# Optimization experiments

Measured on AMD Instinct MI355X. Metric: run time of the kernel, lower is better.

## Reference

```python
import jax, jax.numpy as jnp
import numpy as np

TOKENS, D_IN, D_OUT = 16384, 2048, 2048


def setup_inputs() -> dict:
    key = jax.random.key(0)
    k1, k2, k3 = jax.random.split(key, 3)
    x = jax.random.normal(k1, (TOKENS, D_IN), dtype=jnp.float32)
    # int8 quantized weight, stored transposed as [in_features, out_features]
    weight = jax.random.randint(k2, (D_IN, D_OUT), -128, 128).astype(jnp.int8)
    # per-output-channel dequant scale, shape [1, out_features]
    scale = (jax.random.uniform(k3, (1, D_OUT), dtype=jnp.float32) * 0.01 + 1e-4)
    return {"x": x, "scale": scale, "weight": weight}


def reference(x, scale, weight):
    # x: [N, in], weight: int8 [in, out] (pre-transposed), scale: [1, out]
    tokens = x.shape[:-1]
    xf = x.reshape(-1, x.shape[-1])
    # cast int8 weight to activation dtype, dense matmul, per-channel scale
    y = jnp.matmul(xf, weight.astype(x.dtype)) * scale
    # bias path is dead in the original (`if self.bias:` on a tensor); omitted
    return y.reshape(tokens + (weight.shape[-1],))
```

## Files before the change

### kernel.cpp

```cpp
#include <hip/hip_runtime.h>
#include <cstdint>


#define M_TOK 16384
#define K_DIM 2048
#define N_DIM 2048
#define BK 32

typedef _Float16 f16;
typedef f16 f16x4 __attribute__((ext_vector_type(4)));
typedef f16 f16x8 __attribute__((ext_vector_type(8)));
typedef float f32x4 __attribute__((ext_vector_type(4)));

__global__ void convert_x_kernel(const float* __restrict__ x, f16* __restrict__ xh) {
  const int n4 = (M_TOK * K_DIM) / 4;
  const int stride = gridDim.x * blockDim.x;
  for (int i = blockIdx.x * blockDim.x + threadIdx.x; i < n4; i += stride) {
    float4 v = ((const float4*)x)[i];
    f16x4 h;
    h[0] = (f16)v.x; h[1] = (f16)v.y; h[2] = (f16)v.z; h[3] = (f16)v.w;
    ((f16x4*)xh)[i] = h;
  }
}

__global__ void convert_w_kernel(const int* __restrict__ w, f16* __restrict__ wt) {
  __shared__ f16 tile[64][68];
  const int tid = threadIdx.x;
  const int nb = blockIdx.x * 64;
  const int kb = blockIdx.y * 64;
  const int cq = tid & 15;
  const int rr = tid >> 4;

#pragma unroll
  for (int g = 0; g < 4; ++g) {
    int krow = g * 16 + rr;
    const int* p = w + (size_t)(kb + krow) * N_DIM + nb + cq * 4;
    int4 v = *(const int4*)p;
    tile[cq * 4 + 0][krow] = (f16)(float)v.x;
    tile[cq * 4 + 1][krow] = (f16)(float)v.y;
    tile[cq * 4 + 2][krow] = (f16)(float)v.z;
    tile[cq * 4 + 3][krow] = (f16)(float)v.w;
  }
  __syncthreads();
#pragma unroll
  for (int g = 0; g < 4; ++g) {
    int nrow = g * 16 + rr;
    f16x4 o;
#pragma unroll
    for (int j = 0; j < 4; ++j)
      o[j] = tile[nrow][cq * 4 + j];
    *(f16x4*)(wt + (size_t)(nb + nrow) * K_DIM + kb + cq * 4) = o;
  }
}

__device__ __forceinline__ void async_load16(const void* g, void* l) {
  __builtin_amdgcn_global_load_lds((__attribute__((address_space(1))) void*)g,
                                   (__attribute__((address_space(3))) void*)l,
                                   16, 0, 0);
}

__global__ __launch_bounds__(256) void gemm_f16(
    const f16* __restrict__ xh, const f16* __restrict__ wt,
    const float* __restrict__ scale, float* __restrict__ out) {
  __shared__ __align__(16) f16 sA[128 * BK];
  __shared__ __align__(16) f16 sB[128 * BK];

  const int tid = threadIdx.x;
  const int wave = tid >> 6;
  const int lane = tid & 63;
  const int m0 = blockIdx.y * 128;
  const int n0 = blockIdx.x * 128;
  const int wm = (wave & 1) * 64;
  const int wn = (wave >> 1) * 64;

  const int c0 = wave * 2;
  const int rowA = c0 * 16 + (lane >> 2);
  const int kq8 = (lane & 3) * 8;

  const f16* gA0 = xh + (size_t)(m0 + rowA) * K_DIM + kq8;
  const f16* gA1 = xh + (size_t)(m0 + rowA + 16) * K_DIM + kq8;
  const f16* gB0 = wt + (size_t)(n0 + rowA) * K_DIM + kq8;
  const f16* gB1 = wt + (size_t)(n0 + rowA + 16) * K_DIM + kq8;

  f16* lA0 = sA + c0 * 512;  f16* lA1 = lA0 + 512;
  f16* lB0 = sB + c0 * 512;  f16* lB1 = lB0 + 512;

  const int fr = lane & 15;
  const int fq = (lane >> 4) * 8;

  f32x4 acc[4][4] = {};

  for (int k0 = 0; k0 < K_DIM; k0 += BK) {
    async_load16(gA0 + k0, lA0);
    async_load16(gA1 + k0, lA1);
    async_load16(gB0 + k0, lB0);
    async_load16(gB1 + k0, lB1);
    __syncthreads();

    f16x8 a[4], b[4];
#pragma unroll
    for (int t = 0; t < 4; ++t) {
      a[t] = *(const f16x8*)&sA[(wm + t * 16 + fr) * BK + fq];
      b[t] = *(const f16x8*)&sB[(wn + t * 16 + fr) * BK + fq];
    }
#pragma unroll
    for (int mm = 0; mm < 4; ++mm)
#pragma unroll
      for (int nn = 0; nn < 4; ++nn)
        acc[mm][nn] = __builtin_amdgcn_mfma_f32_16x16x32_f16(a[mm], b[nn], acc[mm][nn], 0, 0, 0);
    __syncthreads();
  }

#pragma unroll
  for (int nn = 0; nn < 4; ++nn) {
    int col = n0 + wn + nn * 16 + fr;
    float s = scale[col];
#pragma unroll
    for (int mm = 0; mm < 4; ++mm) {
      int rbase = m0 + wm + mm * 16 + (lane >> 4) * 4;
      f32x4 v = acc[mm][nn];
#pragma unroll
      for (int r = 0; r < 4; ++r)
        out[(size_t)(rbase + r) * N_DIM + col] = v[r] * s;
    }
  }
}

extern "C" void kernel_launch(void* const* d_in, const int* in_sizes, int n_in,
                              void* d_out, int out_size, void* d_ws, size_t ws_size,
                              hipStream_t stream) {
  const float* x     = (const float*)d_in[0];
  const float* scale = (const float*)d_in[1];
  const int* w       = (const int*)d_in[2];
  float* out         = (float*)d_out;

  char* ws = (char*)d_ws;
  f16* xh = (f16*)ws;
  f16* wt = (f16*)(ws + (size_t)M_TOK * K_DIM * 2);

  convert_x_kernel<<<8192, 256, 0, stream>>>(x, xh);
  convert_w_kernel<<<dim3(N_DIM / 64, K_DIM / 64), 256, 0, stream>>>(w, wt);
  gemm_f16<<<dim3(N_DIM / 128, M_TOK / 128), 256, 0, stream>>>(xh, wt, scale, out);
}
```

Measured before the change: 397.6 us.

## Replace GEMM with 256x256-tile, 8-wave, double-buffered 8-phase pipelined kernel

Rewrites the f16 MFMA GEMM to use 256x256 output tiles with 512 threads, a BK=64 double-buffered LDS ring split into A/B quarter-tiles, and an 8-phase schedule that interleaves async global->LDS loads with MFMA work. It adds XOR-swizzled LDS layout to avoid bank conflicts, explicit vmcnt/lgkmcnt waits, s_setprio around MFMA bursts, and a block-index swizzle for L2 locality. The aim is to hide global load latency and raise MFMA utilisation versus the single-buffered 128x128 kernel. The cost is more complex manual synchronization, a large LDS footprint (128KB) and heavy register pressure from 32 accumulators per lane.

Result: faster. 351.2 us (-11.7%).

```diff
diff --git a/kernel.cpp b/kernel.cpp
--- a/kernel.cpp
+++ b/kernel.cpp
@@ -5,7 +5,6 @@
 #define M_TOK 16384
 #define K_DIM 2048
 #define N_DIM 2048
-#define BK 32
 
 typedef _Float16 f16;
 typedef f16 f16x4 __attribute__((ext_vector_type(4)));
@@ -59,71 +58,142 @@
                                    16, 0, 0);
 }
 
-__global__ __launch_bounds__(256) void gemm_f16(
+#define FENCE() asm volatile("" ::: "memory")
+#define BAR()   do { FENCE(); __builtin_amdgcn_s_barrier(); FENCE(); } while (0)
+#define LGKM0() asm volatile("s_waitcnt lgkmcnt(0)" ::: "memory")
+#define VMCNT_6() asm volatile("s_waitcnt vmcnt(6)" ::: "memory")
+#define VMCNT_0() asm volatile("s_waitcnt vmcnt(0)" ::: "memory")
+
+__global__ __launch_bounds__(512, 2) void gemm_8ph(
     const f16* __restrict__ xh, const f16* __restrict__ wt,
     const float* __restrict__ scale, float* __restrict__ out) {
-  __shared__ __align__(16) f16 sA[128 * BK];
-  __shared__ __align__(16) f16 sB[128 * BK];
-
-  const int tid = threadIdx.x;
-  const int wave = tid >> 6;
+  __shared__ __align__(16) f16 sm[2][4][128 * 64];
+
+  const int tid  = threadIdx.x;
+  const int wid  = tid >> 6;
   const int lane = tid & 63;
-  const int m0 = blockIdx.y * 128;
-  const int n0 = blockIdx.x * 128;
-  const int wm = (wave & 1) * 64;
-  const int wn = (wave >> 1) * 64;
-
-  const int c0 = wave * 2;
-  const int rowA = c0 * 16 + (lane >> 2);
-  const int kq8 = (lane & 3) * 8;
-
-  const f16* gA0 = xh + (size_t)(m0 + rowA) * K_DIM + kq8;
-  const f16* gA1 = xh + (size_t)(m0 + rowA + 16) * K_DIM + kq8;
-  const f16* gB0 = wt + (size_t)(n0 + rowA) * K_DIM + kq8;
-  const f16* gB1 = wt + (size_t)(n0 + rowA + 16) * K_DIM + kq8;
-
-  f16* lA0 = sA + c0 * 512;  f16* lA1 = lA0 + 512;
-  f16* lB0 = sB + c0 * 512;  f16* lB1 = lB0 + 512;
-
+  const int wr = wid >> 2;
+  const int wc = wid & 3;
   const int fr = lane & 15;
-  const int fq = (lane >> 4) * 8;
-
-  f32x4 acc[4][4] = {};
-
-  for (int k0 = 0; k0 < K_DIM; k0 += BK) {
-    async_load16(gA0 + k0, lA0);
-    async_load16(gA1 + k0, lA1);
-    async_load16(gB0 + k0, lB0);
-    async_load16(gB1 + k0, lB1);
-    __syncthreads();
-
-    f16x8 a[4], b[4];
-#pragma unroll
-    for (int t = 0; t < 4; ++t) {
-      a[t] = *(const f16x8*)&sA[(wm + t * 16 + fr) * BK + fq];
-      b[t] = *(const f16x8*)&sB[(wn + t * 16 + fr) * BK + fq];
-    }
-#pragma unroll
-    for (int mm = 0; mm < 4; ++mm)
-#pragma unroll
-      for (int nn = 0; nn < 4; ++nn)
-        acc[mm][nn] = __builtin_amdgcn_mfma_f32_16x16x32_f16(a[mm], b[nn], acc[mm][nn], 0, 0, 0);
-    __syncthreads();
-  }
-
-#pragma unroll
-  for (int nn = 0; nn < 4; ++nn) {
-    int col = n0 + wn + nn * 16 + fr;
-    float s = scale[col];
-#pragma unroll
-    for (int mm = 0; mm < 4; ++mm) {
-      int rbase = m0 + wm + mm * 16 + (lane >> 4) * 4;
-      f32x4 v = acc[mm][nn];
+  const int kq = lane >> 4;
+
+  const int bid = blockIdx.x;
+  const int swz = (bid & 7) * 64 + (bid >> 3);
+  const int n0 = (swz & 7) * 256;
+  const int m0 = (swz >> 3) * 256;
+
+  const int l8   = lane >> 3;
+  const int slot = (lane & 7) ^ l8;
+  const int c0   = wid * 2;
+  const int row0 = c0 * 8 + l8;
+  const int row1 = row0 + 8;
+
+  const f16* gA0 = xh + (size_t)(m0 + (row0 >> 6) * 128 + (row0 & 63)) * K_DIM + slot * 8;
+  const f16* gA1 = xh + (size_t)(m0 + (row1 >> 6) * 128 + (row1 & 63)) * K_DIM + slot * 8;
+  const f16* gB0 = wt + (size_t)(n0 + (row0 >> 5) * 64 + (row0 & 31)) * K_DIM + slot * 8;
+  const f16* gB1 = wt + (size_t)(n0 + (row1 >> 5) * 64 + (row1 & 31)) * K_DIM + slot * 8;
+
+#define STAGE_A(buf, mh, koff) do { \
+    async_load16(gA0 + (mh) * 64 * K_DIM + (koff), &sm[buf][mh][c0 * 512]); \
+    async_load16(gA1 + (mh) * 64 * K_DIM + (koff), &sm[buf][mh][c0 * 512 + 512]); \
+  } while (0)
+#define STAGE_B(buf, nh, koff) do { \
+    async_load16(gB0 + (nh) * 32 * K_DIM + (koff), &sm[buf][2 + (nh)][c0 * 512]); \
+    async_load16(gB1 + (nh) * 32 * K_DIM + (koff), &sm[buf][2 + (nh)][c0 * 512 + 512]); \
+  } while (0)
+
+  const int kx0 = (kq * 8) ^ ((fr & 7) * 8);
+  const int kx1 = (32 + kq * 8) ^ ((fr & 7) * 8);
+
+  f16x8 a[4][2];
+  f16x8 b[2][2][2];
+  f32x4 acc[8][4] = {};
+
+#define LDA(buf, mh) do { \
+    const f16* base_ = &sm[buf][mh][(wr * 64 + fr) * 64]; \
+    _Pragma("unroll") for (int mi_ = 0; mi_ < 4; ++mi_) { \
+      a[mi_][0] = *(const f16x8*)(base_ + mi_ * 1024 + kx0); \
+      a[mi_][1] = *(const f16x8*)(base_ + mi_ * 1024 + kx1); \
+    } } while (0)
+#define LDB(buf, nh) do { \
+    const f16* base_ = &sm[buf][2 + (nh)][(wc * 32 + fr) * 64]; \
+    _Pragma("unroll") for (int ni_ = 0; ni_ < 2; ++ni_) { \
+      b[nh][ni_][0] = *(const f16x8*)(base_ + ni_ * 1024 + kx0); \
+      b[nh][ni_][1] = *(const f16x8*)(base_ + ni_ * 1024 + kx1); \
+    } } while (0)
+#define MMA(mh, nh) do { \
+    __builtin_amdgcn_s_setprio(1); \
+    _Pragma("unroll") for (int mi_ = 0; mi_ < 4; ++mi_) \
+    _Pragma("unroll") for (int ni_ = 0; ni_ < 2; ++ni_) { \
+      acc[(mh)*4+mi_][(nh)*2+ni_] = __builtin_amdgcn_mfma_f32_16x16x32_f16( \
+          a[mi_][0], b[nh][ni_][0], acc[(mh)*4+mi_][(nh)*2+ni_], 0, 0, 0); \
+      acc[(mh)*4+mi_][(nh)*2+ni_] = __builtin_amdgcn_mfma_f32_16x16x32_f16( \
+          a[mi_][1], b[nh][ni_][1], acc[(mh)*4+mi_][(nh)*2+ni_], 0, 0, 0); \
+    } \
+    __builtin_amdgcn_s_setprio(0); } while (0)
+
+  STAGE_A(0, 0, 0); STAGE_B(0, 0, 0); STAGE_B(0, 1, 0); STAGE_A(0, 1, 0);
+  STAGE_A(1, 0, 64); STAGE_B(1, 0, 64); STAGE_B(1, 1, 64);
+  VMCNT_6();
+  BAR();
+
+#pragma unroll 1
+  for (int i = 0; i < 15; ++i) {
+    const int k0 = i * 128;
+    LDA(0, 0); LDB(0, 0); STAGE_A(1, 1, k0 + 64);
+    BAR(); LGKM0(); MMA(0, 0); BAR();
+    LDB(0, 1); STAGE_A(0, 0, k0 + 128);
+    BAR(); LGKM0(); MMA(0, 1); BAR();
+    LDA(0, 1); STAGE_B(0, 0, k0 + 128);
+    BAR(); LGKM0(); MMA(1, 0); BAR();
+    STAGE_B(0, 1, k0 + 128);
+    BAR(); MMA(1, 1); VMCNT_6(); BAR();
+    LDA(1, 0); LDB(1, 0); STAGE_A(0, 1, k0 + 128);
+    BAR(); LGKM0(); MMA(0, 0); BAR();
+    LDB(1, 1); STAGE_A(1, 0, k0 + 192);
+    BAR(); LGKM0(); MMA(0, 1); BAR();
+    LDA(1, 1); STAGE_B(1, 0, k0 + 192);
+    BAR(); LGKM0(); MMA(1, 0); BAR();
+    STAGE_B(1, 1, k0 + 192);
+    BAR(); MMA(1, 1); VMCNT_6(); BAR();
+  }
+
+  {
+    const int k0 = 15 * 128;
+    LDA(0, 0); LDB(0, 0); STAGE_A(1, 1, k0 + 64);
+    BAR(); LGKM0(); MMA(0, 0); BAR();
+    LDB(0, 1);
+    BAR(); LGKM0(); MMA(0, 1); BAR();
+    LDA(0, 1);
+    BAR(); LGKM0(); MMA(1, 0); BAR();
+    BAR(); MMA(1, 1); VMCNT_0(); BAR();
+    LDA(1, 0); LDB(1, 0);
+    BAR(); LGKM0(); MMA(0, 0); BAR();
+    LDB(1, 1);
+    BAR(); LGKM0(); MMA(0, 1); BAR();
+    LDA(1, 1);
+    BAR(); LGKM0(); MMA(1, 0); BAR();
+    MMA(1, 1);
+  }
+
+#pragma unroll
+  for (int ni = 0; ni < 4; ++ni) {
+    const int col = n0 + wc * 64 + (ni >> 1) * 32 + (ni & 1) * 16 + fr;
+    const float s = scale[col];
+#pragma unroll
+    for (int mi = 0; mi < 8; ++mi) {
+      const int rbase = m0 + wr * 128 + (mi >> 2) * 64 + (mi & 3) * 16 + kq * 4;
+      f32x4 v = acc[mi][ni];
 #pragma unroll
       for (int r = 0; r < 4; ++r)
         out[(size_t)(rbase + r) * N_DIM + col] = v[r] * s;
     }
   }
+#undef STAGE_A
+#undef STAGE_B
+#undef LDA
+#undef LDB
+#undef MMA
 }
 
 extern "C" void kernel_launch(void* const* d_in, const int* in_sizes, int n_in,
@@ -140,5 +210,5 @@
 
   convert_x_kernel<<<8192, 256, 0, stream>>>(x, xh);
   convert_w_kernel<<<dim3(N_DIM / 64, K_DIM / 64), 256, 0, stream>>>(w, wt);
-  gemm_f16<<<dim3(N_DIM / 128, M_TOK / 128), 256, 0, stream>>>(xh, wt, scale, out);
-}
+  gemm_8ph<<<dim3((N_DIM / 256) * (M_TOK / 256)), 512, 0, stream>>>(xh, wt, scale, out);
+}
```
